# Performance work log

Hardware: AMD Instinct MI355X
Metric: run time of the kernel (lower is better)

The kernel has to match this reference:

```python
import jax, jax.numpy as jnp
import numpy as np

H, C = 8, 32          # heads, channels per head; H*C = 256 triggers the LN branch
N_NODES = 30000       # nodes per node type
N_EDGES = 100000      # edges per edge type
N_TYPES = 6           # hardwired edge types (all src = Package_Name)
D_IN = 128            # raw input feature dim (Package_Name stays at 128)
LRELU_SLOPE = 0.2     # PyG GATConv default negative_slope


def _segment_softmax(e, dst, n):
    # softmax of per-edge logits e [E,H] grouped by destination node
    m = jax.ops.segment_max(e, dst, num_segments=n)
    ex = jnp.exp(e - m[dst])
    den = jax.ops.segment_sum(ex, dst, num_segments=n)
    return ex / (den[dst] + 1e-16)


def _gat(x_src, x_tgt, src, dst, Ws, Wd, a_s, a_d, b):
    # bipartite GATConv, concat heads, no self loops, no edge features
    hs = (x_src @ Ws).reshape(-1, H, C)   # [Ns,H,C]
    hd = (x_tgt @ Wd).reshape(-1, H, C)   # [Nt,H,C]
    es = jnp.einsum('nhc,hc->nh', hs, a_s)
    ed = jnp.einsum('nhc,hc->nh', hd, a_d)
    e = jax.nn.leaky_relu(es[src] + ed[dst], negative_slope=LRELU_SLOPE)  # [E,H]
    n = x_tgt.shape[0]
    alpha = _segment_softmax(e, dst, n)                                   # [E,H]
    msg = hs[src] * alpha[:, :, None]                                     # [E,H,C]
    out = jax.ops.segment_sum(msg, dst, num_segments=n).reshape(n, H * C) + b
    return out, alpha


def _ln_relu(x, g, b):
    mu = x.mean(-1, keepdims=True)
    var = ((x - mu) ** 2).mean(-1, keepdims=True)
    return jax.nn.relu((x - mu) / jnp.sqrt(var + 1e-5) * g + b)


def setup_inputs() -> dict:
    key = jax.random.key(0)
    ks = jax.random.split(key, 16)
    s = 0.05
    return {
        'x_pkg': jax.random.normal(ks[0], (N_NODES, D_IN), jnp.float32),
        'x_tgt': jax.random.normal(ks[1], (N_TYPES, N_NODES, D_IN), jnp.float32),
        'edge_index': jax.random.randint(ks[2], (N_TYPES, 2, N_EDGES), 0, N_NODES, jnp.int32),
        'W1_src': jax.random.normal(ks[3], (N_TYPES, D_IN, H * C), jnp.float32) * s,
        'W1_dst': jax.random.normal(ks[4], (N_TYPES, D_IN, H * C), jnp.float32) * s,
        'att1_src': jax.random.normal(ks[5], (N_TYPES, H, C), jnp.float32) * s,
        'att1_dst': jax.random.normal(ks[6], (N_TYPES, H, C), jnp.float32) * s,
        'b1': jnp.zeros((N_TYPES, H * C), jnp.float32),
        'W2_src': jax.random.normal(ks[7], (N_TYPES, D_IN, H * C), jnp.float32) * s,
        'W2_dst': jax.random.normal(ks[8], (N_TYPES, H * C, H * C), jnp.float32) * s,
        'att2_src': jax.random.normal(ks[9], (N_TYPES, H, C), jnp.float32) * s,
        'att2_dst': jax.random.normal(ks[10], (N_TYPES, H, C), jnp.float32) * s,
        'b2': jnp.zeros((N_TYPES, H * C), jnp.float32),
        'gamma': jnp.ones((N_TYPES, H * C), jnp.float32),
        'beta': jnp.zeros((N_TYPES, H * C), jnp.float32),
        'Wc': jax.random.normal(ks[11], (N_TYPES * H * C + D_IN, 1), jnp.float32) * s,
        'bc': jnp.zeros((1,), jnp.float32),
    }


def reference(x_pkg, x_tgt, edge_index, W1_src, W1_dst, att1_src, att1_dst, b1,
              W2_src, W2_dst, att2_src, att2_dst, b2, gamma, beta, Wc, bc):
    def layer(xt, ei, Ws, Wd, a_s, a_d, bb):
        return _gat(x_pkg, xt, ei[0], ei[1], Ws, Wd, a_s, a_d, bb)

    vlayer = jax.vmap(layer, in_axes=(0, 0, 0, 0, 0, 0, 0))

    # layer 1: Package_Name -> each of 6 target types; Package_Name itself unchanged
    out1, _ = vlayer(x_tgt, edge_index, W1_src, W1_dst, att1_src, att1_dst, b1)
    x1 = jax.vmap(_ln_relu)(out1, gamma, beta)   # module reuses ln1 after both layers

    # layer 2: src features are still the raw 128-d Package_Name features
    out2, alpha2 = vlayer(x1, edge_index, W2_src, W2_dst, att2_src, att2_dst, b2)
    x2 = jax.vmap(_ln_relu)(out2, gamma, beta)

    # global mean pool per node type, concat (6 targets then Package_Name), classify
    pooled = jnp.concatenate([x2.mean(axis=1).reshape(-1), x_pkg.mean(axis=0)])
    logits = pooled @ Wc[:, 0] + bc[0]
    return logits, alpha2
```

## Files before the change

### kernel.cpp

```cpp
#include <hip/hip_runtime.h>
#include <hip/hip_bf16.h>
#include <cstddef>

#define N_NODES 30000
#define N_EDGES 100000
#define N_TYPES 6
#define D_IN 128
#define HC 256
#define NH 8
#define CH 32

typedef __attribute__((ext_vector_type(8))) unsigned short ushort8_t;
typedef __attribute__((ext_vector_type(4))) unsigned short ushort4_t;
typedef __attribute__((ext_vector_type(8))) __bf16 bf16x8;
typedef __attribute__((ext_vector_type(4))) float floatx4;

#define FG_GRID (N_NODES / 4)

__device__ inline unsigned short f2bf(float f) {
    unsigned u = __float_as_uint(f);
    u += 0x7fffu + ((u >> 16) & 1u);
    return (unsigned short)(u >> 16);
}
__device__ inline float bf2f(unsigned short u) {
    return __uint_as_float(((unsigned)u) << 16);
}

__global__ void zero4(float4* __restrict__ p, int n4) {
    int g = blockIdx.x * blockDim.x + threadIdx.x;
    if (g < n4) p[g] = make_float4(0.f, 0.f, 0.f, 0.f);
}
__global__ void zero_i(int* __restrict__ p, int n) {
    int g = blockIdx.x * blockDim.x + threadIdx.x;
    if (g < n) p[g] = 0;
}
__global__ void to_bf16(const float* __restrict__ x, unsigned short* __restrict__ o, int n4) {
    int g = blockIdx.x * blockDim.x + threadIdx.x;
    if (g >= n4) return;
    float4 v = ((const float4*)x)[g];
    ushort4_t p;
    p[0] = f2bf(v.x); p[1] = f2bf(v.y); p[2] = f2bf(v.z); p[3] = f2bf(v.w);
    *(ushort4_t*)&o[(size_t)g * 4] = p;
}

__global__ void hist_all(const int* __restrict__ ei, int* __restrict__ counts) {
    int t = blockIdx.y;
    int e = blockIdx.x * 256 + threadIdx.x;
    if (e < N_EDGES)
        atomicAdd(&counts[t * N_NODES + ei[(size_t)t * 2 * N_EDGES + N_EDGES + e]], 1);
}

#define SCAN_T 1024
#define SCAN_C 30
__global__ __launch_bounds__(1024) void scan_all(const int* __restrict__ counts_g,
                                                 int* __restrict__ row_ptr_g,
                                                 int* __restrict__ cursor_g) {
    int t = blockIdx.x;
    const int* counts = counts_g + t * N_NODES;
    int* row_ptr = row_ptr_g + t * (N_NODES + 1);
    int* cursor = cursor_g + t * N_NODES;
    __shared__ int part[SCAN_T];
    int tid = threadIdx.x;
    int base = tid * SCAN_C;
    int loc[SCAN_C];
    int s = 0;
    #pragma unroll
    for (int i = 0; i < SCAN_C; ++i) {
        int idx = base + i;
        int v = (idx < N_NODES) ? counts[idx] : 0;
        loc[i] = s; s += v;
    }
    part[tid] = s;
    __syncthreads();
    int tot = s;
    for (int d = 1; d < SCAN_T; d <<= 1) {
        int v = (tid >= d) ? part[tid - d] : 0;
        __syncthreads();
        part[tid] += v;
        __syncthreads();
    }
    int off = part[tid] - tot;
    #pragma unroll
    for (int i = 0; i < SCAN_C; ++i) {
        int idx = base + i;
        if (idx < N_NODES) { int r = off + loc[i]; row_ptr[idx] = r; cursor[idx] = r; }
    }
    if (tid == SCAN_T - 1) row_ptr[N_NODES] = part[SCAN_T - 1];
}

__global__ void fill_all(const int* __restrict__ ei, int* __restrict__ cursor,
                         int* __restrict__ elist) {
    int t = blockIdx.y;
    int e = blockIdx.x * 256 + threadIdx.x;
    if (e < N_EDGES) {
        const int* src = ei + (size_t)t * 2 * N_EDGES;
        const int* dst = src + N_EDGES;
        int pos = atomicAdd(&cursor[t * N_NODES + dst[e]], 1);
        elist[t * N_EDGES + pos] = src[e];
    }
}

__global__ void att_weight_all(const float* __restrict__ W1d, const float* __restrict__ a1d,
                               const float* __restrict__ W2d, const float* __restrict__ a2d,
                               float* __restrict__ wd1, float* __restrict__ wd2) {
    int g = blockIdx.x * blockDim.x + threadIdx.x;
    const int per_t = (D_IN + HC) * NH;
    if (g >= N_TYPES * per_t) return;
    int t = g / per_t, r = g % per_t;
    if (r < D_IN * NH) {
        int k = r >> 3, h = r & 7;
        const float* wr = W1d + (size_t)t * D_IN * HC + (size_t)k * HC + h * CH;
        const float* ar = a1d + t * HC + h * CH;
        float s = 0.f;
        #pragma unroll
        for (int c = 0; c < CH; ++c) s += wr[c] * ar[c];
        wd1[t * D_IN * NH + h * D_IN + k] = s;
    } else {
        r -= D_IN * NH;
        int k = r >> 3, h = r & 7;
        const float* wr = W2d + (size_t)t * HC * HC + (size_t)k * HC + h * CH;
        const float* ar = a2d + t * HC + h * CH;
        float s = 0.f;
        #pragma unroll
        for (int c = 0; c < CH; ++c) s += wr[c] * ar[c];
        wd2[t * HC * NH + h * HC + k] = s;
    }
}

__global__ __launch_bounds__(256) void wt_prep(const float* __restrict__ W1s,
                                               const float* __restrict__ W2s,
                                               unsigned short* __restrict__ Wt) {
    const int j = blockIdx.z;
    const float* W = (j < 6) ? W1s + (size_t)j * D_IN * HC
                             : W2s + (size_t)(j - 6) * D_IN * HC;
    const int n0 = blockIdx.x * 64;
    const int k0 = blockIdx.y * 32;
    __shared__ unsigned short tile[32][71];
    const int t = threadIdx.x;
    {
        const int k = t >> 3, n = (t & 7) * 8;
        const float4 a = *(const float4*)&W[(size_t)(k0 + k) * HC + n0 + n];
        const float4 b = *(const float4*)&W[(size_t)(k0 + k) * HC + n0 + n + 4];
        tile[k][n + 0] = f2bf(a.x); tile[k][n + 1] = f2bf(a.y);
        tile[k][n + 2] = f2bf(a.z); tile[k][n + 3] = f2bf(a.w);
        tile[k][n + 4] = f2bf(b.x); tile[k][n + 5] = f2bf(b.y);
        tile[k][n + 6] = f2bf(b.z); tile[k][n + 7] = f2bf(b.w);
    }
    __syncthreads();
    {
        const int n = t >> 2, k = (t & 3) * 8;
        ushort8_t v;
        #pragma unroll
        for (int q = 0; q < 8; ++q) v[q] = tile[k + q][n];
        *(ushort8_t*)&Wt[((size_t)j * HC + n0 + n) * D_IN + k0 + k] = v;
    }
}

__global__ __launch_bounds__(256) void ed1_all(const float* __restrict__ x_tgt,
                                               const float* __restrict__ wd1,
                                               float* __restrict__ ed1g) {
    const int t = blockIdx.y;
    const int lane = threadIdx.x & 63;
    const int wv = threadIdx.x >> 6;
    const int n8 = lane >> 3, h = lane & 7;
    const int node = blockIdx.x * 32 + wv * 8 + n8;
    if (node >= N_NODES) return;
    const float* xr = x_tgt + ((size_t)t * N_NODES + node) * D_IN;
    const float* wp = wd1 + t * D_IN * NH + h * D_IN;
    float acc = 0.f;
    #pragma unroll
    for (int k = 0; k < D_IN; k += 4) {
        const float4 x4 = *(const float4*)&xr[k];
        const float4 w4 = *(const float4*)&wp[k];
        acc += x4.x * w4.x + x4.y * w4.y + x4.z * w4.z + x4.w * w4.w;
    }
    ed1g[((size_t)t * N_NODES + node) * NH + h] = acc;
}

__global__ __launch_bounds__(256) void gemm_all(const unsigned short* __restrict__ A,
                                                const unsigned short* __restrict__ Wt,
                                                const float* __restrict__ att1,
                                                const float* __restrict__ att2,
                                                unsigned short* __restrict__ hs_all,
                                                float* __restrict__ es_all) {
    const int j = blockIdx.z;
    const unsigned short* B = Wt + (size_t)j * HC * D_IN;
    const float* att = (j < 6) ? att1 + j * HC : att2 + (j - 6) * HC;
    unsigned short* Cp = hs_all + (size_t)j * N_NODES * HC;
    float* e_out = es_all + (size_t)j * N_NODES * NH;

    __shared__ __align__(16) unsigned short As[64 * 136];
    __shared__ __align__(16) unsigned short Bs[128 * 136];

    const int tid = threadIdx.x;
    const int w = tid >> 6;
    const int lane = tid & 63;
    const int col = lane & 15;
    const int quad = lane >> 4;
    const int m0 = blockIdx.x * 64;
    const int n0 = blockIdx.y * 128;

    {
        const int r = tid >> 2;
        const int kc = (tid & 3) * 8;
        const int gm = m0 + r;
        #pragma unroll
        for (int c = 0; c < 4; ++c) {
            ushort8_t v = (ushort8_t){0, 0, 0, 0, 0, 0, 0, 0};
            if (gm < N_NODES) v = *(const ushort8_t*)&A[(size_t)gm * D_IN + kc + c * 32];
            *(ushort8_t*)&As[r * 136 + kc + c * 32] = v;
        }
    }
    {
        const int r = tid >> 1;
        const int ks = (tid & 1) * 64;
        const unsigned short* br = &B[(size_t)(n0 + r) * D_IN + ks];
        #pragma unroll
        for (int q = 0; q < 8; ++q) {
            ushort8_t v = *(const ushort8_t*)&br[q * 8];
            *(ushort8_t*)&Bs[r * 136 + ks + q * 8] = v;
        }
    }
    __syncthreads();

    floatx4 acc[8];
    #pragma unroll
    for (int ct = 0; ct < 8; ++ct) acc[ct] = (floatx4){0.f, 0.f, 0.f, 0.f};

    #pragma unroll
    for (int ks = 0; ks < 4; ++ks) {
        ushort8_t araw = *(const ushort8_t*)&As[(w * 16 + col) * 136 + ks * 32 + quad * 8];
        bf16x8 af = __builtin_bit_cast(bf16x8, araw);
        #pragma unroll
        for (int ct = 0; ct < 8; ++ct) {
            ushort8_t braw = *(const ushort8_t*)&Bs[(ct * 16 + col) * 136 + ks * 32 + quad * 8];
            bf16x8 bf = __builtin_bit_cast(bf16x8, braw);
            acc[ct] = __builtin_amdgcn_mfma_f32_16x16x32_bf16(af, bf, acc[ct], 0, 0, 0);
        }
    }

    float attv[8];
    #pragma unroll
    for (int ct = 0; ct < 8; ++ct) attv[ct] = att[n0 + ct * 16 + col];
    const int hbase = n0 >> 5;
    #pragma unroll
    for (int r = 0; r < 4; ++r) {
        float h0v = acc[0][r] * attv[0] + acc[1][r] * attv[1];
        float h1v = acc[2][r] * attv[2] + acc[3][r] * attv[3];
        float h2v = acc[4][r] * attv[4] + acc[5][r] * attv[5];
        float h3v = acc[6][r] * attv[6] + acc[7][r] * attv[7];
        #pragma unroll
        for (int off = 1; off < 16; off <<= 1) {
            h0v += __shfl_xor(h0v, off);
            h1v += __shfl_xor(h1v, off);
            h2v += __shfl_xor(h2v, off);
            h3v += __shfl_xor(h3v, off);
        }
        if (col == 0) {
            int gm = m0 + w * 16 + quad * 4 + r;
            if (gm < N_NODES)
                *(float4*)&e_out[gm * NH + hbase] = make_float4(h0v, h1v, h2v, h3v);
        }
    }

    __syncthreads();
    unsigned short* Cs = (unsigned short*)Bs;
    #pragma unroll
    for (int ct = 0; ct < 8; ++ct) {
        const int cc = ct * 16 + col;
        #pragma unroll
        for (int r = 0; r < 4; ++r)
            Cs[(w * 16 + quad * 4 + r) * 144 + cc] = f2bf(acc[ct][r]);
    }
    __syncthreads();
    {
        const int r = tid >> 2;
        const int c0 = (tid & 3) * 32;
        const int gm = m0 + r;
        if (gm < N_NODES) {
            #pragma unroll
            for (int q = 0; q < 4; ++q) {
                ushort8_t v = *(const ushort8_t*)&Cs[r * 144 + c0 + q * 8];
                *(ushort8_t*)&Cp[(size_t)gm * HC + n0 + c0 + q * 8] = v;
            }
        }
    }
}

__device__ inline void edge4(const float* __restrict__ es,
                             const unsigned short* __restrict__ hs,
                             int s_pre, int i, int cm,
                             int h_l, int lane, float ed_mine,
                             float& den, float4& acc) {
    const int i1 = (i + 1 < cm) ? i + 1 : cm;
    const int i2 = (i + 2 < cm) ? i + 2 : cm;
    const int i3 = (i + 3 < cm) ? i + 3 : cm;
    const int s0 = __shfl(s_pre, i);
    const int s1 = __shfl(s_pre, i1);
    const int s2 = __shfl(s_pre, i2);
    const int s3 = __shfl(s_pre, i3);
    float q0 = es[s0 * NH + h_l];
    float q1 = es[s1 * NH + h_l];
    float q2 = es[s2 * NH + h_l];
    float q3 = es[s3 * NH + h_l];
    const ushort4_t v0 = *(const ushort4_t*)&hs[(size_t)s0 * HC + lane * 4];
    const ushort4_t v1 = *(const ushort4_t*)&hs[(size_t)s1 * HC + lane * 4];
    const ushort4_t v2 = *(const ushort4_t*)&hs[(size_t)s2 * HC + lane * 4];
    const ushort4_t v3 = *(const ushort4_t*)&hs[(size_t)s3 * HC + lane * 4];
    q0 += ed_mine; q0 = (q0 >= 0.f) ? q0 : 0.2f * q0;
    q1 += ed_mine; q1 = (q1 >= 0.f) ? q1 : 0.2f * q1;
    q2 += ed_mine; q2 = (q2 >= 0.f) ? q2 : 0.2f * q2;
    q3 += ed_mine; q3 = (q3 >= 0.f) ? q3 : 0.2f * q3;
    const float x0 = __expf(q0);
    const float x1 = (i + 1 <= cm) ? __expf(q1) : 0.f;
    const float x2 = (i + 2 <= cm) ? __expf(q2) : 0.f;
    const float x3 = (i + 3 <= cm) ? __expf(q3) : 0.f;
    den += (x0 + x1) + (x2 + x3);
    acc.x += x0 * bf2f(v0[0]) + x1 * bf2f(v1[0]) + x2 * bf2f(v2[0]) + x3 * bf2f(v3[0]);
    acc.y += x0 * bf2f(v0[1]) + x1 * bf2f(v1[1]) + x2 * bf2f(v2[1]) + x3 * bf2f(v3[1]);
    acc.z += x0 * bf2f(v0[2]) + x1 * bf2f(v1[2]) + x2 * bf2f(v2[2]) + x3 * bf2f(v3[2]);
    acc.w += x0 * bf2f(v0[3]) + x1 * bf2f(v1[3]) + x2 * bf2f(v2[3]) + x3 * bf2f(v3[3]);
}

__device__ inline void edge1(const float* __restrict__ es,
                             const unsigned short* __restrict__ hs,
                             int s, int h_l, int lane, float ed_mine,
                             float& den, float4& acc) {
    float x = es[s * NH + h_l] + ed_mine;
    x = (x >= 0.f) ? x : 0.2f * x;
    const float ex = __expf(x);
    den += ex;
    const ushort4_t hv = *(const ushort4_t*)&hs[(size_t)s * HC + lane * 4];
    acc.x += ex * bf2f(hv[0]); acc.y += ex * bf2f(hv[1]);
    acc.z += ex * bf2f(hv[2]); acc.w += ex * bf2f(hv[3]);
}

__global__ __launch_bounds__(256) void fused_gather_all(
        const int* __restrict__ row_ptr_g, const int* __restrict__ elist_g,
        const float* __restrict__ es_all, const float* __restrict__ ed1g,
        const unsigned short* __restrict__ hs_all,
        const float* __restrict__ b1, const float* __restrict__ b2,
        const float* __restrict__ gamma, const float* __restrict__ beta,
        const float* __restrict__ wd2,
        float* __restrict__ ed2g_all, float* __restrict__ deng_all,
        float* __restrict__ ppart) {
    const int t = blockIdx.y;
    const int* row_ptr = row_ptr_g + t * (N_NODES + 1);
    const int* elist = elist_g + t * N_EDGES;
    const float* es1 = es_all + (size_t)t * N_NODES * NH;
    const float* es2 = es_all + (size_t)(6 + t) * N_NODES * NH;
    const unsigned short* hs1 = hs_all + (size_t)t * N_NODES * HC;
    const unsigned short* hs2 = hs_all + (size_t)(6 + t) * N_NODES * HC;
    const float* gam = gamma + t * HC;
    const float* bet = beta + t * HC;
    const float* w2 = wd2 + t * HC * NH;
    float* ed2g = ed2g_all + (size_t)t * N_NODES * NH;
    float* deng = deng_all + (size_t)t * N_NODES * NH;

    const int lane = threadIdx.x & 63;
    const int w = threadIdx.x >> 6;
    const int d = blockIdx.x * 4 + w;
    const int h_l = lane >> 3;

    const float ed_mine = ed1g[((size_t)t * N_NODES + d) * NH + h_l];
    const int e0 = row_ptr[d], e1n = row_ptr[d + 1];
    const int cnt = e1n - e0;
    int s_pre = 0;
    if (lane < cnt) s_pre = elist[e0 + lane];

    float den1 = 0.f, den2 = 0.f;
    float4 acc1 = make_float4(0.f, 0.f, 0.f, 0.f);
    float4 acc2 = make_float4(0.f, 0.f, 0.f, 0.f);

    float q20, q21, q22, q23;
    ushort4_t v20, v21, v22, v23;
    const bool fast = (cnt > 0) && (cnt <= 4);

    if (fast) {
        const int cm = cnt - 1;
        const int s0 = __shfl(s_pre, 0);
        const int s1 = __shfl(s_pre, (1 < cm) ? 1 : cm);
        const int s2 = __shfl(s_pre, (2 < cm) ? 2 : cm);
        const int s3 = __shfl(s_pre, cm);
        float q10 = es1[s0 * NH + h_l];
        float q11 = es1[s1 * NH + h_l];
        float q12 = es1[s2 * NH + h_l];
        float q13 = es1[s3 * NH + h_l];
        const ushort4_t v10 = *(const ushort4_t*)&hs1[(size_t)s0 * HC + lane * 4];
        const ushort4_t v11 = *(const ushort4_t*)&hs1[(size_t)s1 * HC + lane * 4];
        const ushort4_t v12 = *(const ushort4_t*)&hs1[(size_t)s2 * HC + lane * 4];
        const ushort4_t v13 = *(const ushort4_t*)&hs1[(size_t)s3 * HC + lane * 4];
        q20 = es2[s0 * NH + h_l];
        q21 = es2[s1 * NH + h_l];
        q22 = es2[s2 * NH + h_l];
        q23 = es2[s3 * NH + h_l];
        v20 = *(const ushort4_t*)&hs2[(size_t)s0 * HC + lane * 4];
        v21 = *(const ushort4_t*)&hs2[(size_t)s1 * HC + lane * 4];
        v22 = *(const ushort4_t*)&hs2[(size_t)s2 * HC + lane * 4];
        v23 = *(const ushort4_t*)&hs2[(size_t)s3 * HC + lane * 4];
        q10 += ed_mine; q10 = (q10 >= 0.f) ? q10 : 0.2f * q10;
        q11 += ed_mine; q11 = (q11 >= 0.f) ? q11 : 0.2f * q11;
        q12 += ed_mine; q12 = (q12 >= 0.f) ? q12 : 0.2f * q12;
        q13 += ed_mine; q13 = (q13 >= 0.f) ? q13 : 0.2f * q13;
        const float x0 = __expf(q10);
        const float x1 = (cnt > 1) ? __expf(q11) : 0.f;
        const float x2 = (cnt > 2) ? __expf(q12) : 0.f;
        const float x3 = (cnt > 3) ? __expf(q13) : 0.f;
        den1 = (x0 + x1) + (x2 + x3);
        acc1.x = x0 * bf2f(v10[0]) + x1 * bf2f(v11[0]) + x2 * bf2f(v12[0]) + x3 * bf2f(v13[0]);
        acc1.y = x0 * bf2f(v10[1]) + x1 * bf2f(v11[1]) + x2 * bf2f(v12[1]) + x3 * bf2f(v13[1]);
        acc1.z = x0 * bf2f(v10[2]) + x1 * bf2f(v11[2]) + x2 * bf2f(v12[2]) + x3 * bf2f(v13[2]);
        acc1.w = x0 * bf2f(v10[3]) + x1 * bf2f(v11[3]) + x2 * bf2f(v12[3]) + x3 * bf2f(v13[3]);
    } else if (cnt > 0) {
        const int c1 = (cnt < 64) ? cnt : 64;
        const int cm = c1 - 1;
        for (int i = 0; i < c1; i += 4)
            edge4(es1, hs1, s_pre, i, cm, h_l, lane, ed_mine, den1, acc1);
        if (cnt > 64)
            for (int ii = e0 + 64; ii < e1n; ++ii)
                edge1(es1, hs1, elist[ii], h_l, lane, ed_mine, den1, acc1);
    }

    const float inv1 = 1.f / (den1 + 1e-16f);
    const float4 bv1 = *(const float4*)&b1[t * HC + lane * 4];
    acc1.x = acc1.x * inv1 + bv1.x; acc1.y = acc1.y * inv1 + bv1.y;
    acc1.z = acc1.z * inv1 + bv1.z; acc1.w = acc1.w * inv1 + bv1.w;

    float s1 = acc1.x + acc1.y + acc1.z + acc1.w;
    float s2 = acc1.x * acc1.x + acc1.y * acc1.y + acc1.z * acc1.z + acc1.w * acc1.w;
    #pragma unroll
    for (int off = 1; off < 64; off <<= 1) { s1 += __shfl_xor(s1, off); s2 += __shfl_xor(s2, off); }
    const float mu = s1 * (1.f / 256.f);
    const float var = s2 * (1.f / 256.f) - mu * mu;
    const float rstd = rsqrtf(var + 1e-5f);
    const float4 g4 = *(const float4*)&gam[lane * 4];
    const float4 b4 = *(const float4*)&bet[lane * 4];
    const float ya0 = fmaxf((acc1.x - mu) * rstd * g4.x + b4.x, 0.f);
    const float ya1 = fmaxf((acc1.y - mu) * rstd * g4.y + b4.y, 0.f);
    const float ya2 = fmaxf((acc1.z - mu) * rstd * g4.z + b4.z, 0.f);
    const float ya3 = fmaxf((acc1.w - mu) * rstd * g4.w + b4.w, 0.f);

    __shared__ __align__(16) float ya_s[4][256];
    {
        const int c0 = lane * 4;
        const int widx = (c0 & ~31) | ((c0 & 31) ^ ((lane >> 3) << 2));
        *(float4*)&ya_s[w][widx] = make_float4(ya0, ya1, ya2, ya3);
    }
    const int k8 = lane >> 3;
    const int hh = lane & 7;
    const float* w2h = w2 + hh * HC;
    float e2 = 0.f;
    #pragma unroll
    for (int jj = 0; jj < 8; ++jj) {
        const int idx = k8 * 32 + ((jj * 4) ^ (k8 << 2));
        const float4 y = *(const float4*)&ya_s[w][idx];
        const float4 wv = *(const float4*)&w2h[k8 * 32 + jj * 4];
        e2 += y.x * wv.x + y.y * wv.y + y.z * wv.z + y.w * wv.w;
    }
    e2 += __shfl_xor(e2, 8);
    e2 += __shfl_xor(e2, 16);
    e2 += __shfl_xor(e2, 32);
    if (lane < 8) ed2g[d * NH + lane] = e2;
    const float ed2_mine = __shfl(e2, h_l);

    if (fast) {
        q20 += ed2_mine; q20 = (q20 >= 0.f) ? q20 : 0.2f * q20;
        q21 += ed2_mine; q21 = (q21 >= 0.f) ? q21 : 0.2f * q21;
        q22 += ed2_mine; q22 = (q22 >= 0.f) ? q22 : 0.2f * q22;
        q23 += ed2_mine; q23 = (q23 >= 0.f) ? q23 : 0.2f * q23;
        const float x0 = __expf(q20);
        const float x1 = (cnt > 1) ? __expf(q21) : 0.f;
        const float x2 = (cnt > 2) ? __expf(q22) : 0.f;
        const float x3 = (cnt > 3) ? __expf(q23) : 0.f;
        den2 = (x0 + x1) + (x2 + x3);
        acc2.x = x0 * bf2f(v20[0]) + x1 * bf2f(v21[0]) + x2 * bf2f(v22[0]) + x3 * bf2f(v23[0]);
        acc2.y = x0 * bf2f(v20[1]) + x1 * bf2f(v21[1]) + x2 * bf2f(v22[1]) + x3 * bf2f(v23[1]);
        acc2.z = x0 * bf2f(v20[2]) + x1 * bf2f(v21[2]) + x2 * bf2f(v22[2]) + x3 * bf2f(v23[2]);
        acc2.w = x0 * bf2f(v20[3]) + x1 * bf2f(v21[3]) + x2 * bf2f(v22[3]) + x3 * bf2f(v23[3]);
    } else if (cnt > 0) {
        const int c1 = (cnt < 64) ? cnt : 64;
        const int cm = c1 - 1;
        for (int i = 0; i < c1; i += 4)
            edge4(es2, hs2, s_pre, i, cm, h_l, lane, ed2_mine, den2, acc2);
        if (cnt > 64)
            for (int ii = e0 + 64; ii < e1n; ++ii)
                edge1(es2, hs2, elist[ii], h_l, lane, ed2_mine, den2, acc2);
    }

    if ((lane & 7) == 0) deng[d * NH + h_l] = den2;
    const float inv2 = 1.f / (den2 + 1e-16f);
    const float4 bv2 = *(const float4*)&b2[t * HC + lane * 4];
    acc2.x = acc2.x * inv2 + bv2.x; acc2.y = acc2.y * inv2 + bv2.y;
    acc2.z = acc2.z * inv2 + bv2.z; acc2.w = acc2.w * inv2 + bv2.w;

    float t1 = acc2.x + acc2.y + acc2.z + acc2.w;
    float t2 = acc2.x * acc2.x + acc2.y * acc2.y + acc2.z * acc2.z + acc2.w * acc2.w;
    #pragma unroll
    for (int off = 1; off < 64; off <<= 1) { t1 += __shfl_xor(t1, off); t2 += __shfl_xor(t2, off); }
    const float mu2 = t1 * (1.f / 256.f);
    const float var2 = t2 * (1.f / 256.f) - mu2 * mu2;
    const float rstd2 = rsqrtf(var2 + 1e-5f);
    float4 pool;
    pool.x = fmaxf((acc2.x - mu2) * rstd2 * g4.x + b4.x, 0.f);
    pool.y = fmaxf((acc2.y - mu2) * rstd2 * g4.y + b4.y, 0.f);
    pool.z = fmaxf((acc2.z - mu2) * rstd2 * g4.z + b4.z, 0.f);
    pool.w = fmaxf((acc2.w - mu2) * rstd2 * g4.w + b4.w, 0.f);

    __shared__ __align__(16) float sacc[4][260];
    *(float4*)&sacc[w][lane * 4] = pool;
    __syncthreads();
    const int tid = threadIdx.x;
    float tot = sacc[0][tid] + sacc[1][tid] + sacc[2][tid] + sacc[3][tid];
    ppart[((size_t)t * FG_GRID + blockIdx.x) * HC + tid] = tot;
}

__global__ __launch_bounds__(256) void pool_reduce_all(const float* __restrict__ ppart,
                                                       float* __restrict__ psums) {
    int t = blockIdx.y;
    const float* part = ppart + (size_t)t * FG_GRID * HC;
    int tid = threadIdx.x;
    float acc = 0.f;
    for (int b = blockIdx.x; b < FG_GRID; b += gridDim.x)
        acc += part[(size_t)b * HC + tid];
    atomicAdd(&psums[t * HC + tid], acc);
}

__global__ __launch_bounds__(256) void alpha_all(const int* __restrict__ ei,
                          const float* __restrict__ es_all,
                          const float* __restrict__ ed2g_all,
                          const float* __restrict__ deng_all,
                          float* __restrict__ out) {
    int t = blockIdx.y;
    int e = blockIdx.x * 256 + threadIdx.x;
    if (e >= N_EDGES) return;
    const int* src = ei + (size_t)t * 2 * N_EDGES;
    const int* dst = src + N_EDGES;
    const int s = src[e], d = dst[e];
    const float* esp = es_all + (size_t)(6 + t) * N_NODES * NH + (size_t)s * NH;
    const float* edp = ed2g_all + (size_t)t * N_NODES * NH + (size_t)d * NH;
    const float* dnp = deng_all + (size_t)t * N_NODES * NH + (size_t)d * NH;
    const float4 ea = *(const float4*)esp;
    const float4 eb = *(const float4*)(esp + 4);
    const float4 da = *(const float4*)edp;
    const float4 db = *(const float4*)(edp + 4);
    const float4 na = *(const float4*)dnp;
    const float4 nb = *(const float4*)(dnp + 4);
    float x[8];
    x[0] = ea.x + da.x; x[1] = ea.y + da.y; x[2] = ea.z + da.z; x[3] = ea.w + da.w;
    x[4] = eb.x + db.x; x[5] = eb.y + db.y; x[6] = eb.z + db.z; x[7] = eb.w + db.w;
    float n[8] = {na.x, na.y, na.z, na.w, nb.x, nb.y, nb.z, nb.w};
    float* op = out + (size_t)t * N_EDGES * NH + (size_t)e * NH;
    #pragma unroll
    for (int h = 0; h < 8; ++h) {
        float v = x[h];
        v = (v >= 0.f) ? v : 0.2f * v;
        op[h] = __expf(v) / (n[h] + 1e-16f);
    }
}

__global__ __launch_bounds__(256) void pkg_accum(const float* __restrict__ x, float* __restrict__ sums) {
    int tid = threadIdx.x;
    int col = tid & 127;
    int rof = tid >> 7;
    float acc = 0.f;
    for (int r = blockIdx.x * 2 + rof; r < N_NODES; r += gridDim.x * 2)
        acc += x[(size_t)r * D_IN + col];
    atomicAdd(&sums[col], acc);
}

__global__ __launch_bounds__(256) void logits_k(const float* __restrict__ psums,
                                                const float* __restrict__ ksums,
                                                const float* __restrict__ Wc,
                                                const float* __restrict__ bc,
                                                float* __restrict__ out) {
    int tid = threadIdx.x;
    const float inv = 1.f / (float)N_NODES;
    float acc = 0.f;
    for (int i = tid; i < N_TYPES * HC; i += 256) acc += psums[i] * inv * Wc[i];
    if (tid < D_IN) acc += ksums[tid] * inv * Wc[N_TYPES * HC + tid];
    #pragma unroll
    for (int off = 32; off; off >>= 1) acc += __shfl_down(acc, off);
    __shared__ float w[4];
    if ((tid & 63) == 0) w[tid >> 6] = acc;
    __syncthreads();
    if (tid == 0) out[0] = w[0] + w[1] + w[2] + w[3] + bc[0];
}

static inline void zf(float* p, int n, hipStream_t stream) {
    int n4 = (n + 3) >> 2;
    zero4<<<(n4 + 255) / 256, 256, 0, stream>>>((float4*)p, n4);
}

extern "C" void kernel_launch(void* const* d_in, const int* in_sizes, int n_in,
                              void* d_out, int out_size, void* d_ws, size_t ws_size,
                              hipStream_t stream) {
    const float* x_pkg    = (const float*)d_in[0];
    const float* x_tgt    = (const float*)d_in[1];
    const int*   ei       = (const int*)d_in[2];
    const float* W1_src   = (const float*)d_in[3];
    const float* W1_dst   = (const float*)d_in[4];
    const float* att1_src = (const float*)d_in[5];
    const float* att1_dst = (const float*)d_in[6];
    const float* b1       = (const float*)d_in[7];
    const float* W2_src   = (const float*)d_in[8];
    const float* W2_dst   = (const float*)d_in[9];
    const float* att2_src = (const float*)d_in[10];
    const float* att2_dst = (const float*)d_in[11];
    const float* b2       = (const float*)d_in[12];
    const float* gamma    = (const float*)d_in[13];
    const float* beta     = (const float*)d_in[14];
    const float* Wc       = (const float*)d_in[15];
    const float* bc       = (const float*)d_in[16];
    float* out = (float*)d_out;

    char* wsb = (char*)d_ws;
    unsigned short* xpkg_bf = (unsigned short*)wsb;
    unsigned short* hs_all  = xpkg_bf + (size_t)N_NODES * D_IN;
    float* es_all   = (float*)(hs_all + (size_t)12 * N_NODES * HC);
    float* ed2g_all = es_all + (size_t)12 * N_NODES * NH;
    float* deng_all = ed2g_all + (size_t)N_TYPES * N_NODES * NH;
    float* psums    = deng_all + (size_t)N_TYPES * N_NODES * NH;
    float* ksums    = psums + N_TYPES * HC;
    float* wd1      = ksums + D_IN;
    float* wd2      = wd1 + N_TYPES * D_IN * NH;
    unsigned short* Wt = (unsigned short*)(wd2 + N_TYPES * HC * NH);
    float* ed1g     = (float*)(Wt + (size_t)12 * HC * D_IN);
    float* ppart    = ed1g + (size_t)N_TYPES * N_NODES * NH;
    int* counts  = (int*)(ppart + (size_t)N_TYPES * FG_GRID * HC);
    int* row_ptr = counts + N_TYPES * N_NODES;
    int* cursor  = row_ptr + N_TYPES * (N_NODES + 1);
    int* elist   = cursor + N_TYPES * N_NODES;

    dim3 egrid((N_EDGES + 255) / 256, N_TYPES);

    zf(psums, N_TYPES * HC + D_IN, stream);
    pkg_accum<<<256, 256, 0, stream>>>(x_pkg, ksums);
    {
        int tot = N_TYPES * (D_IN + HC) * NH;
        att_weight_all<<<(tot + 255) / 256, 256, 0, stream>>>(W1_dst, att1_dst, W2_dst, att2_dst, wd1, wd2);
    }
    {
        dim3 g(4, 4, 12);
        wt_prep<<<g, 256, 0, stream>>>(W1_src, W2_src, Wt);
    }
    {
        dim3 g((N_NODES + 31) / 32, N_TYPES);
        ed1_all<<<g, 256, 0, stream>>>(x_tgt, wd1, ed1g);
    }
    to_bf16<<<((N_NODES * D_IN / 4) + 255) / 256, 256, 0, stream>>>(x_pkg, xpkg_bf, N_NODES * D_IN / 4);
    zero_i<<<(N_TYPES * N_NODES + 255) / 256, 256, 0, stream>>>(counts, N_TYPES * N_NODES);
    hist_all<<<egrid, 256, 0, stream>>>(ei, counts);
    scan_all<<<N_TYPES, SCAN_T, 0, stream>>>(counts, row_ptr, cursor);
    fill_all<<<egrid, 256, 0, stream>>>(ei, cursor, elist);

    {
        dim3 g((N_NODES + 63) / 64, 2, 12);
        gemm_all<<<g, 256, 0, stream>>>(xpkg_bf, Wt, att1_src, att2_src,
                                        hs_all, es_all);
    }

    {
        dim3 g(FG_GRID, N_TYPES);
        fused_gather_all<<<g, 256, 0, stream>>>(row_ptr, elist, es_all, ed1g, hs_all,
                                                b1, b2, gamma, beta, wd2,
                                                ed2g_all, deng_all, ppart);
    }
    {
        dim3 g(64, N_TYPES);
        pool_reduce_all<<<g, 256, 0, stream>>>(ppart, psums);
    }
    {
        dim3 g((N_EDGES + 255) / 256, N_TYPES);
        alpha_all<<<g, 256, 0, stream>>>(ei, es_all, ed2g_all, deng_all, out + 1);
    }

    logits_k<<<1, 256, 0, stream>>>(psums, ksums, Wc, bc, out);
}
```

Baseline: 840.5 us.

## Fuse layer-2 attention alpha output into gather kernel via CSR edge-origin map

```diff
diff --git a/kernel.cpp b/kernel.cpp
--- a/kernel.cpp
+++ b/kernel.cpp
@@ -89,7 +89,7 @@
 }
 
 __global__ void fill_all(const int* __restrict__ ei, int* __restrict__ cursor,
-                         int* __restrict__ elist) {
+                         int* __restrict__ elist, int* __restrict__ eorig) {
     int t = blockIdx.y;
     int e = blockIdx.x * 256 + threadIdx.x;
     if (e < N_EDGES) {
@@ -97,6 +97,7 @@
         const int* dst = src + N_EDGES;
         int pos = atomicAdd(&cursor[t * N_NODES + dst[e]], 1);
         elist[t * N_EDGES + pos] = src[e];
+        eorig[t * N_EDGES + pos] = e;
     }
 }
 
@@ -337,16 +338,18 @@
 
 __global__ __launch_bounds__(256) void fused_gather_all(
         const int* __restrict__ row_ptr_g, const int* __restrict__ elist_g,
+        const int* __restrict__ eorig_g,
         const float* __restrict__ es_all, const float* __restrict__ ed1g,
         const unsigned short* __restrict__ hs_all,
         const float* __restrict__ b1, const float* __restrict__ b2,
         const float* __restrict__ gamma, const float* __restrict__ beta,
         const float* __restrict__ wd2,
-        float* __restrict__ ed2g_all, float* __restrict__ deng_all,
+        float* __restrict__ alpha_out,
         float* __restrict__ ppart) {
     const int t = blockIdx.y;
     const int* row_ptr = row_ptr_g + t * (N_NODES + 1);
     const int* elist = elist_g + t * N_EDGES;
+    const int* eorig = eorig_g + t * N_EDGES;
     const float* es1 = es_all + (size_t)t * N_NODES * NH;
     const float* es2 = es_all + (size_t)(6 + t) * N_NODES * NH;
     const unsigned short* hs1 = hs_all + (size_t)t * N_NODES * HC;
@@ -354,8 +357,7 @@
     const float* gam = gamma + t * HC;
     const float* bet = beta + t * HC;
     const float* w2 = wd2 + t * HC * NH;
-    float* ed2g = ed2g_all + (size_t)t * N_NODES * NH;
-    float* deng = deng_all + (size_t)t * N_NODES * NH;
+    float* aout = alpha_out + (size_t)t * N_EDGES * NH;
 
     const int lane = threadIdx.x & 63;
     const int w = threadIdx.x >> 6;
@@ -365,14 +367,18 @@
     const float ed_mine = ed1g[((size_t)t * N_NODES + d) * NH + h_l];
     const int e0 = row_ptr[d], e1n = row_ptr[d + 1];
     const int cnt = e1n - e0;
-    int s_pre = 0;
-    if (lane < cnt) s_pre = elist[e0 + lane];
+    int s_pre = 0, eo_pre = 0;
+    if (lane < cnt) {
+        s_pre = elist[e0 + lane];
+        eo_pre = eorig[e0 + lane];
+    }
 
     float den1 = 0.f, den2 = 0.f;
     float4 acc1 = make_float4(0.f, 0.f, 0.f, 0.f);
     float4 acc2 = make_float4(0.f, 0.f, 0.f, 0.f);
 
     float q20, q21, q22, q23;
+    float ax0 = 0.f, ax1 = 0.f, ax2 = 0.f, ax3 = 0.f;
     ushort4_t v20, v21, v22, v23;
     const bool fast = (cnt > 0) && (cnt <= 4);
 
@@ -460,7 +466,6 @@
     e2 += __shfl_xor(e2, 8);
     e2 += __shfl_xor(e2, 16);
     e2 += __shfl_xor(e2, 32);
-    if (lane < 8) ed2g[d * NH + lane] = e2;
     const float ed2_mine = __shfl(e2, h_l);
 
     if (fast) {
@@ -468,15 +473,15 @@
         q21 += ed2_mine; q21 = (q21 >= 0.f) ? q21 : 0.2f * q21;
         q22 += ed2_mine; q22 = (q22 >= 0.f) ? q22 : 0.2f * q22;
         q23 += ed2_mine; q23 = (q23 >= 0.f) ? q23 : 0.2f * q23;
-        const float x0 = __expf(q20);
-        const float x1 = (cnt > 1) ? __expf(q21) : 0.f;
-        const float x2 = (cnt > 2) ? __expf(q22) : 0.f;
-        const float x3 = (cnt > 3) ? __expf(q23) : 0.f;
-        den2 = (x0 + x1) + (x2 + x3);
-        acc2.x = x0 * bf2f(v20[0]) + x1 * bf2f(v21[0]) + x2 * bf2f(v22[0]) + x3 * bf2f(v23[0]);
-        acc2.y = x0 * bf2f(v20[1]) + x1 * bf2f(v21[1]) + x2 * bf2f(v22[1]) + x3 * bf2f(v23[1]);
-        acc2.z = x0 * bf2f(v20[2]) + x1 * bf2f(v21[2]) + x2 * bf2f(v22[2]) + x3 * bf2f(v23[2]);
-        acc2.w = x0 * bf2f(v20[3]) + x1 * bf2f(v21[3]) + x2 * bf2f(v22[3]) + x3 * bf2f(v23[3]);
+        ax0 = __expf(q20);
+        ax1 = (cnt > 1) ? __expf(q21) : 0.f;
+        ax2 = (cnt > 2) ? __expf(q22) : 0.f;
+        ax3 = (cnt > 3) ? __expf(q23) : 0.f;
+        den2 = (ax0 + ax1) + (ax2 + ax3);
+        acc2.x = ax0 * bf2f(v20[0]) + ax1 * bf2f(v21[0]) + ax2 * bf2f(v22[0]) + ax3 * bf2f(v23[0]);
+        acc2.y = ax0 * bf2f(v20[1]) + ax1 * bf2f(v21[1]) + ax2 * bf2f(v22[1]) + ax3 * bf2f(v23[1]);
+        acc2.z = ax0 * bf2f(v20[2]) + ax1 * bf2f(v21[2]) + ax2 * bf2f(v22[2]) + ax3 * bf2f(v23[2]);
+        acc2.w = ax0 * bf2f(v20[3]) + ax1 * bf2f(v21[3]) + ax2 * bf2f(v22[3]) + ax3 * bf2f(v23[3]);
     } else if (cnt > 0) {
         const int c1 = (cnt < 64) ? cnt : 64;
         const int cm = c1 - 1;
@@ -487,8 +492,42 @@
                 edge1(es2, hs2, elist[ii], h_l, lane, ed2_mine, den2, acc2);
     }
 
-    if ((lane & 7) == 0) deng[d * NH + h_l] = den2;
     const float inv2 = 1.f / (den2 + 1e-16f);
+
+    if (fast) {
+        const int eo0 = __shfl(eo_pre, 0);
+        const int eo1 = __shfl(eo_pre, 1);
+        const int eo2 = __shfl(eo_pre, 2);
+        const int eo3 = __shfl(eo_pre, 3);
+        if ((lane & 7) == 0) {
+            aout[(size_t)eo0 * NH + h_l] = ax0 * inv2;
+            if (cnt > 1) aout[(size_t)eo1 * NH + h_l] = ax1 * inv2;
+            if (cnt > 2) aout[(size_t)eo2 * NH + h_l] = ax2 * inv2;
+            if (cnt > 3) aout[(size_t)eo3 * NH + h_l] = ax3 * inv2;
+        }
+    } else if (cnt > 0) {
+        const int c1 = (cnt < 64) ? cnt : 64;
+        for (int i = 0; i < c1; ++i) {
+            const int si = __shfl(s_pre, i);
+            const int eo = __shfl(eo_pre, i);
+            if ((lane & 7) == 0) {
+                float x = es2[si * NH + h_l] + ed2_mine;
+                x = (x >= 0.f) ? x : 0.2f * x;
+                aout[(size_t)eo * NH + h_l] = __expf(x) * inv2;
+            }
+        }
+        if (cnt > 64)
+            for (int ii = e0 + 64; ii < e1n; ++ii) {
+                const int si = elist[ii];
+                const int eo = eorig[ii];
+                if ((lane & 7) == 0) {
+                    float x = es2[si * NH + h_l] + ed2_mine;
+                    x = (x >= 0.f) ? x : 0.2f * x;
+                    aout[(size_t)eo * NH + h_l] = __expf(x) * inv2;
+                }
+            }
+    }
+
     const float4 bv2 = *(const float4*)&b2[t * HC + lane * 4];
     acc2.x = acc2.x * inv2 + bv2.x; acc2.y = acc2.y * inv2 + bv2.y;
     acc2.z = acc2.z * inv2 + bv2.z; acc2.w = acc2.w * inv2 + bv2.w;
@@ -523,39 +562,6 @@
     for (int b = blockIdx.x; b < FG_GRID; b += gridDim.x)
         acc += part[(size_t)b * HC + tid];
     atomicAdd(&psums[t * HC + tid], acc);
-}
-
-__global__ __launch_bounds__(256) void alpha_all(const int* __restrict__ ei,
-                          const float* __restrict__ es_all,
-                          const float* __restrict__ ed2g_all,
-                          const float* __restrict__ deng_all,
-                          float* __restrict__ out) {
-    int t = blockIdx.y;
-    int e = blockIdx.x * 256 + threadIdx.x;
-    if (e >= N_EDGES) return;
-    const int* src = ei + (size_t)t * 2 * N_EDGES;
-    const int* dst = src + N_EDGES;
-    const int s = src[e], d = dst[e];
-    const float* esp = es_all + (size_t)(6 + t) * N_NODES * NH + (size_t)s * NH;
-    const float* edp = ed2g_all + (size_t)t * N_NODES * NH + (size_t)d * NH;
-    const float* dnp = deng_all + (size_t)t * N_NODES * NH + (size_t)d * NH;
-    const float4 ea = *(const float4*)esp;
-    const float4 eb = *(const float4*)(esp + 4);
-    const float4 da = *(const float4*)edp;
-    const float4 db = *(const float4*)(edp + 4);
-    const float4 na = *(const float4*)dnp;
-    const float4 nb = *(const float4*)(dnp + 4);
-    float x[8];
-    x[0] = ea.x + da.x; x[1] = ea.y + da.y; x[2] = ea.z + da.z; x[3] = ea.w + da.w;
-    x[4] = eb.x + db.x; x[5] = eb.y + db.y; x[6] = eb.z + db.z; x[7] = eb.w + db.w;
-    float n[8] = {na.x, na.y, na.z, na.w, nb.x, nb.y, nb.z, nb.w};
-    float* op = out + (size_t)t * N_EDGES * NH + (size_t)e * NH;
-    #pragma unroll
-    for (int h = 0; h < 8; ++h) {
-        float v = x[h];
-        v = (v >= 0.f) ? v : 0.2f * v;
-        op[h] = __expf(v) / (n[h] + 1e-16f);
-    }
 }
 
 __global__ __launch_bounds__(256) void pkg_accum(const float* __restrict__ x, float* __restrict__ sums) {
@@ -617,9 +623,7 @@
     unsigned short* xpkg_bf = (unsigned short*)wsb;
     unsigned short* hs_all  = xpkg_bf + (size_t)N_NODES * D_IN;
     float* es_all   = (float*)(hs_all + (size_t)12 * N_NODES * HC);
-    float* ed2g_all = es_all + (size_t)12 * N_NODES * NH;
-    float* deng_all = ed2g_all + (size_t)N_TYPES * N_NODES * NH;
-    float* psums    = deng_all + (size_t)N_TYPES * N_NODES * NH;
+    float* psums    = es_all + (size_t)12 * N_NODES * NH;
     float* ksums    = psums + N_TYPES * HC;
     float* wd1      = ksums + D_IN;
     float* wd2      = wd1 + N_TYPES * D_IN * NH;
@@ -630,6 +634,7 @@
     int* row_ptr = counts + N_TYPES * N_NODES;
     int* cursor  = row_ptr + N_TYPES * (N_NODES + 1);
     int* elist   = cursor + N_TYPES * N_NODES;
+    int* eorig   = elist + N_TYPES * N_EDGES;
 
     dim3 egrid((N_EDGES + 255) / 256, N_TYPES);
 
@@ -651,7 +656,7 @@
     zero_i<<<(N_TYPES * N_NODES + 255) / 256, 256, 0, stream>>>(counts, N_TYPES * N_NODES);
     hist_all<<<egrid, 256, 0, stream>>>(ei, counts);
     scan_all<<<N_TYPES, SCAN_T, 0, stream>>>(counts, row_ptr, cursor);
-    fill_all<<<egrid, 256, 0, stream>>>(ei, cursor, elist);
+    fill_all<<<egrid, 256, 0, stream>>>(ei, cursor, elist, eorig);
 
     {
         dim3 g((N_NODES + 63) / 64, 2, 12);
@@ -661,18 +666,14 @@
 
     {
         dim3 g(FG_GRID, N_TYPES);
-        fused_gather_all<<<g, 256, 0, stream>>>(row_ptr, elist, es_all, ed1g, hs_all,
+        fused_gather_all<<<g, 256, 0, stream>>>(row_ptr, elist, eorig, es_all, ed1g, hs_all,
                                                 b1, b2, gamma, beta, wd2,
-                                                ed2g_all, deng_all, ppart);
+                                                out + 1, ppart);
     }
     {
         dim3 g(64, N_TYPES);
         pool_reduce_all<<<g, 256, 0, stream>>>(ppart, psums);
     }
-    {
-        dim3 g((N_EDGES + 255) / 256, N_TYPES);
-        alpha_all<<<g, 256, 0, stream>>>(ei, es_all, ed2g_all, deng_all, out + 1);
-    }
 
     logits_k<<<1, 256, 0, stream>>>(psums, ksums, Wc, bc, out);
 }
```

After: 872.8 us. 3.8% more time.
